# Performance work log

Measured on AMD Instinct MI355X. Metric: run time of the kernel, lower is better.

## Reference

```python
import jax, jax.numpy as jnp
import numpy as np

B, N, D, P = 4, 16384, 128, 100


def setup_inputs() -> dict:
    key = jax.random.key(0)
    k1, k2, k3 = jax.random.split(key, 3)
    x = jax.random.normal(k1, (B, N, D), dtype=jnp.float32)
    y = jax.random.normal(k2, (B, N, D), dtype=jnp.float32)
    thetas = jax.random.normal(k3, (P, D), dtype=jnp.float32)
    return {"x": x, "y": y, "thetas": thetas}


def reference(x, y, thetas):
    # Sliced OT (the branch taken since B*N*N*4 bytes >> memory limit).
    n_proj = thetas.shape[0]
    # F.normalize(theta, dim=0) per projection direction (eps clamp 1e-12)
    norms = jnp.maximum(jnp.linalg.norm(thetas, axis=-1, keepdims=True), 1e-12)
    thetas = thetas / norms  # (P, d)

    # Project all points onto all directions: (P, B, N)
    x_proj = jnp.einsum('bnd,pd->pbn', x, thetas)
    y_proj = jnp.einsum('bnd,pd->pbn', y, thetas)

    # torch: sort y_proj; scatter y_sorted back to original order of x via
    # x_indices = argsort(x_proj). Equivalent: transported_proj[n] =
    # y_sorted[rank_of_x_proj[n]], with rank = argsort(argsort(.)).
    y_sorted = jnp.sort(y_proj, axis=-1)
    ranks = jnp.argsort(jnp.argsort(x_proj, axis=-1), axis=-1)
    transported_proj = jnp.take_along_axis(y_sorted, ranks, axis=-1)  # (P, B, N)

    # Accumulate (transported_proj - x_proj) * theta over projections.
    transported = jnp.einsum('pbn,pd->bnd', transported_proj - x_proj, thetas)
    return x + transported / n_proj
```

## Files before the change

### kernel.cpp

```cpp
#include <hip/hip_runtime.h>
#include <hip/hip_bf16.h>

#define B_    4
#define N_    16384
#define D_    128
#define P_    100
#define BN_   65536
#define PBN_  6553600
#define PPAD  112
#define KPAD  128
#define NBIN  4096

typedef __attribute__((ext_vector_type(8))) short short8;
typedef __attribute__((ext_vector_type(4))) float floatx4;

__device__ __forceinline__ unsigned short f2b(float f) {
    unsigned u = __float_as_uint(f);
    return (unsigned short)((u + 0x7FFFu + ((u >> 16) & 1u)) >> 16);
}
__device__ __forceinline__ float b2f(unsigned short h) {
    return __uint_as_float(((unsigned)h) << 16);
}

__global__ void k_norm(const float* __restrict__ th,
                       unsigned short* __restrict__ thb,
                       unsigned short* __restrict__ thbT) {
    int p = blockIdx.x;
    int d = threadIdx.x;
    float v = 0.f;
    if (p < P_) v = th[p * D_ + d];
    float s = v * v;
    #pragma unroll
    for (int o = 32; o > 0; o >>= 1) s += __shfl_down(s, o, 64);
    __shared__ float red[2];
    if ((d & 63) == 0) red[d >> 6] = s;
    __syncthreads();
    float norm = fmaxf(sqrtf(red[0] + red[1]), 1e-12f);
    unsigned short r = f2b(v / norm);
    if (p < PPAD) thb[p * D_ + d] = r;
    thbT[d * KPAD + p] = r;
}

__global__ __launch_bounds__(256) void k_proj(
    const float* __restrict__ x, const float* __restrict__ y,
    const unsigned short* __restrict__ thb,
    unsigned short* __restrict__ xp, unsigned short* __restrict__ yp) {
    __shared__ unsigned short smem[32640];
    unsigned short* th_s = smem;
    unsigned short* xs   = smem + 15232;
    unsigned short* ys   = xs + 8704;
    unsigned short* bufx = xs;
    unsigned short* bufy = bufx + 8064;
    const int tid  = threadIdx.x;
    const int w    = tid >> 6;
    const int lane = tid & 63;
    const int n    = lane & 15;
    const int quad = lane >> 4;
    const int row0 = blockIdx.x * 64;

    for (int g = tid; g < 1792; g += 256) {
        int r = g >> 4, c = (g & 15) << 3;
        *(uint4*)(th_s + r * 136 + c) = *(const uint4*)(thb + r * D_ + c);
    }
    for (int g = tid; g < 2048; g += 256) {
        int r = g >> 5, c = (g & 31) << 2;
        float4 vx = *(const float4*)(x + (size_t)(row0 + r) * D_ + c);
        float4 vy = *(const float4*)(y + (size_t)(row0 + r) * D_ + c);
        *(ushort4*)(xs + r * 136 + c) =
            make_ushort4(f2b(vx.x), f2b(vx.y), f2b(vx.z), f2b(vx.w));
        *(ushort4*)(ys + r * 136 + c) =
            make_ushort4(f2b(vy.x), f2b(vy.y), f2b(vy.z), f2b(vy.w));
    }
    __syncthreads();

    short8 bx[4], by[4];
    #pragma unroll
    for (int ks = 0; ks < 4; ++ks) {
        bx[ks] = *(const short8*)(xs + (w * 16 + n) * 136 + ks * 32 + quad * 8);
        by[ks] = *(const short8*)(ys + (w * 16 + n) * 136 + ks * 32 + quad * 8);
    }
    __syncthreads();

    #pragma unroll
    for (int pt = 0; pt < 7; ++pt) {
        floatx4 accx = {0.f, 0.f, 0.f, 0.f};
        floatx4 accy = {0.f, 0.f, 0.f, 0.f};
        #pragma unroll
        for (int ks = 0; ks < 4; ++ks) {
            short8 a = *(const short8*)(th_s + (pt * 16 + n) * 136 + ks * 32 + quad * 8);
            accx = __builtin_amdgcn_mfma_f32_16x16x32_bf16(a, bx[ks], accx, 0, 0, 0);
            accy = __builtin_amdgcn_mfma_f32_16x16x32_bf16(a, by[ks], accy, 0, 0, 0);
        }
        #pragma unroll
        for (int reg = 0; reg < 4; ++reg) {
            int p = pt * 16 + quad * 4 + reg;
            bufx[p * 72 + w * 16 + n] = f2b(accx[reg]);
            bufy[p * 72 + w * 16 + n] = f2b(accy[reg]);
        }
    }
    __syncthreads();

    for (int g = tid; g < 896; g += 256) {
        int p = g >> 3, c = (g & 7) << 3;
        *(uint4*)(xp + (size_t)p * BN_ + row0 + c) = *(const uint4*)(bufx + p * 72 + c);
        *(uint4*)(yp + (size_t)p * BN_ + row0 + c) = *(const uint4*)(bufy + p * 72 + c);
    }
}

__device__ __forceinline__ int binof(float v) {
    int k = (int)((v + 8.0f) * 256.0f);
    return k < 0 ? 0 : (k > NBIN - 1 ? NBIN - 1 : k);
}

__device__ __forceinline__ void scan4(unsigned* hist, volatile unsigned* wsum, int t) {
    unsigned v[4], run = 0;
    #pragma unroll
    for (int i = 0; i < 4; ++i) { unsigned h = hist[t * 4 + i]; v[i] = run; run += h; }
    const int lane = t & 63, w = t >> 6;
    unsigned inc = run;
    #pragma unroll
    for (int off = 1; off < 64; off <<= 1) {
        unsigned nbr = __shfl_up(inc, off, 64);
        if (lane >= off) inc += nbr;
    }
    if (lane == 63) wsum[w] = inc;
    __syncthreads();
    if (t == 0) {
        unsigned r2 = 0;
        #pragma unroll
        for (int i = 0; i < 16; ++i) { unsigned h = wsum[i]; wsum[i] = r2; r2 += h; }
    }
    __syncthreads();
    unsigned base = wsum[w] + (inc - run);
    #pragma unroll
    for (int i = 0; i < 4; ++i) hist[t * 4 + i] = base + v[i];
}

__global__ __launch_bounds__(1024, 4) void k_sortdiff(
    const unsigned short* __restrict__ xp, const unsigned short* __restrict__ yp,
    unsigned short* __restrict__ diff) {
    __shared__ unsigned hist[NBIN];
    __shared__ unsigned short ysort[N_];
    __shared__ unsigned wsum[16];
    const size_t base = (size_t)blockIdx.x * N_ + (size_t)threadIdx.x * 16;
    const int t = threadIdx.x;

    unsigned yw[8], xw[8];
    {
        uint4 a = *(const uint4*)(yp + base), b = *(const uint4*)(yp + base + 8);
        yw[0]=a.x; yw[1]=a.y; yw[2]=a.z; yw[3]=a.w;
        yw[4]=b.x; yw[5]=b.y; yw[6]=b.z; yw[7]=b.w;
        uint4 c = *(const uint4*)(xp + base), d = *(const uint4*)(xp + base + 8);
        xw[0]=c.x; xw[1]=c.y; xw[2]=c.z; xw[3]=c.w;
        xw[4]=d.x; xw[5]=d.y; xw[6]=d.z; xw[7]=d.w;
    }

    #pragma unroll
    for (int i = 0; i < 4; ++i) hist[t + i * 1024] = 0;
    __syncthreads();

    unsigned jy[8], jx[8];
    #pragma unroll
    for (int k = 0; k < 8; ++k) {
        unsigned j0 = atomicAdd(&hist[binof(b2f((unsigned short)(yw[k] & 0xffff)))], 1u);
        unsigned j1 = atomicAdd(&hist[binof(b2f((unsigned short)(yw[k] >> 16)))], 1u);
        jy[k] = (j0 & 0xffffu) | (j1 << 16);
        unsigned i0 = atomicAdd(&hist[binof(b2f((unsigned short)(xw[k] & 0xffff)))], 0x10000u);
        unsigned i1 = atomicAdd(&hist[binof(b2f((unsigned short)(xw[k] >> 16)))], 0x10000u);
        jx[k] = (i0 >> 16) | (i1 & 0xffff0000u);
    }
    __syncthreads();
    scan4(hist, wsum, t);
    __syncthreads();

    #pragma unroll
    for (int k = 0; k < 8; ++k) {
        unsigned short e0 = (unsigned short)(yw[k] & 0xffff);
        unsigned short e1 = (unsigned short)(yw[k] >> 16);
        ysort[(hist[binof(b2f(e0))] & 0xffffu) + (jy[k] & 0xffffu)] = e0;
        ysort[(hist[binof(b2f(e1))] & 0xffffu) + (jy[k] >> 16)]     = e1;
        unsigned r0 = (hist[binof(b2f((unsigned short)(xw[k] & 0xffff)))] >> 16) + (jx[k] & 0xffffu);
        unsigned r1 = (hist[binof(b2f((unsigned short)(xw[k] >> 16)))] >> 16) + (jx[k] >> 16);
        jx[k] = r0 | (r1 << 16);
    }
    __syncthreads();

    unsigned ow[8];
    #pragma unroll
    for (int k = 0; k < 8; ++k) {
        float x0 = b2f((unsigned short)(xw[k] & 0xffff));
        float x1 = b2f((unsigned short)(xw[k] >> 16));
        unsigned short d0 = f2b(b2f(ysort[jx[k] & 0xffffu]) - x0);
        unsigned short d1 = f2b(b2f(ysort[jx[k] >> 16]) - x1);
        ow[k] = (unsigned)d0 | ((unsigned)d1 << 16);
    }
    *(uint4*)(diff + base)     = make_uint4(ow[0], ow[1], ow[2], ow[3]);
    *(uint4*)(diff + base + 8) = make_uint4(ow[4], ow[5], ow[6], ow[7]);
}

__global__ __launch_bounds__(256) void k_comb(
    const float* __restrict__ x, const unsigned short* __restrict__ diff,
    const unsigned short* __restrict__ thbT, float* __restrict__ out) {
    __shared__ unsigned short ths[128 * 136];
    __shared__ unsigned Lp[64 * 68];
    const int tid  = threadIdx.x;
    const int w    = tid >> 6;
    const int lane = tid & 63;
    const int n16  = lane & 15;
    const int quad = lane >> 4;
    const int row0 = blockIdx.x * 64;

    for (int g = tid; g < 2048; g += 256) {
        int r = g >> 4, c = (g & 15) << 3;
        *(uint4*)(ths + r * 136 + c) = *(const uint4*)(thbT + r * KPAD + c);
    }
    for (int g = tid; g < 952; g += 256) Lp[50 * 68 + g] = 0;
    for (int g = tid; g < 400; g += 256) {
        int p2 = g >> 3, rg = (g & 7) << 3;
        uint4 a = *(const uint4*)(diff + (size_t)(2 * p2) * BN_ + row0 + rg);
        uint4 b = *(const uint4*)(diff + (size_t)(2 * p2 + 1) * BN_ + row0 + rg);
        unsigned* dst = Lp + p2 * 68 + rg;
        dst[0] = (a.x & 0xffffu) | (b.x << 16);
        dst[1] = (a.x >> 16)     | (b.x & 0xffff0000u);
        dst[2] = (a.y & 0xffffu) | (b.y << 16);
        dst[3] = (a.y >> 16)     | (b.y & 0xffff0000u);
        dst[4] = (a.z & 0xffffu) | (b.z << 16);
        dst[5] = (a.z >> 16)     | (b.z & 0xffff0000u);
        dst[6] = (a.w & 0xffffu) | (b.w << 16);
        dst[7] = (a.w >> 16)     | (b.w & 0xffff0000u);
    }
    __syncthreads();

    const int r = w * 16 + n16;
    short8 af[4];
    #pragma unroll
    for (int ks = 0; ks < 4; ++ks) {
        union { unsigned u[4]; short8 v; } tu;
        #pragma unroll
        for (int m = 0; m < 4; ++m)
            tu.u[m] = Lp[(ks * 16 + quad * 4 + m) * 68 + r];
        af[ks] = tu.v;
    }

    floatx4 acc[8];
    #pragma unroll
    for (int nt = 0; nt < 8; ++nt) {
        acc[nt] = (floatx4){0.f, 0.f, 0.f, 0.f};
        #pragma unroll
        for (int ks = 0; ks < 4; ++ks) {
            short8 b = *(const short8*)(ths + (nt * 16 + n16) * 136 + ks * 32 + quad * 8);
            acc[nt] = __builtin_amdgcn_mfma_f32_16x16x32_bf16(af[ks], b, acc[nt], 0, 0, 0);
        }
    }

    const float invP = 1.0f / (float)P_;
    const size_t rbase = (size_t)(row0 + w * 16 + quad * 4) * D_ + n16;
    #pragma unroll
    for (int nt = 0; nt < 8; ++nt)
        #pragma unroll
        for (int reg = 0; reg < 4; ++reg) {
            size_t o = rbase + (size_t)reg * D_ + nt * 16;
            out[o] = fmaf(acc[nt][reg], invP, x[o]);
        }
}

extern "C" void kernel_launch(void* const* d_in, const int* in_sizes, int n_in,
                              void* d_out, int out_size, void* d_ws, size_t ws_size,
                              hipStream_t stream) {
    const float* x  = (const float*)d_in[0];
    const float* y  = (const float*)d_in[1];
    const float* th = (const float*)d_in[2];
    float* out = (float*)d_out;
    char*  wsb = (char*)d_ws;

    unsigned short* thb  = (unsigned short*)wsb;
    unsigned short* thbT = (unsigned short*)(wsb + 32768);
    unsigned short* xpb  = (unsigned short*)(wsb + 65536);
    unsigned short* ypb  = xpb + PBN_;

    k_norm<<<128, 128, 0, stream>>>(th, thb, thbT);
    k_proj<<<BN_ / 64, 256, 0, stream>>>(x, y, thb, xpb, ypb);
    k_sortdiff<<<P_ * B_, 1024, 0, stream>>>(xpb, ypb, xpb);
    k_comb<<<BN_ / 64, 256, 0, stream>>>(x, xpb, thbT, out);
}
```

Measured before the change: 154.4 us.

## Load projection inputs straight to registers and halve sort block size

k_proj now reads x and y rows directly from global memory into registers in MFMA operand layout, skipping the shared-memory staging pass and its barrier. This shrinks its LDS footprint and adds a two-blocks-per-CU launch bound. k_sortdiff moves from 1024 to 512 threads, with each thread handling 32 elements in coalesced strided chunks and an 8-bin-per-thread scan. The trade-off is more registers per thread and less latency hiding per block in the sort, and uncoalesced-ish row reads in the projection.

```diff
diff --git a/kernel.cpp b/kernel.cpp
--- a/kernel.cpp
+++ b/kernel.cpp
@@ -41,16 +41,13 @@
     thbT[d * KPAD + p] = r;
 }
 
-__global__ __launch_bounds__(256) void k_proj(
+__global__ __launch_bounds__(256, 2) void k_proj(
     const float* __restrict__ x, const float* __restrict__ y,
     const unsigned short* __restrict__ thb,
     unsigned short* __restrict__ xp, unsigned short* __restrict__ yp) {
-    __shared__ unsigned short smem[32640];
-    unsigned short* th_s = smem;
-    unsigned short* xs   = smem + 15232;
-    unsigned short* ys   = xs + 8704;
-    unsigned short* bufx = xs;
-    unsigned short* bufy = bufx + 8064;
+    __shared__ unsigned short th_s[15232];
+    __shared__ unsigned short bufx[8064];
+    __shared__ unsigned short bufy[8064];
     const int tid  = threadIdx.x;
     const int w    = tid >> 6;
     const int lane = tid & 63;
@@ -62,22 +59,30 @@
         int r = g >> 4, c = (g & 15) << 3;
         *(uint4*)(th_s + r * 136 + c) = *(const uint4*)(thb + r * D_ + c);
     }
-    for (int g = tid; g < 2048; g += 256) {
-        int r = g >> 5, c = (g & 31) << 2;
-        float4 vx = *(const float4*)(x + (size_t)(row0 + r) * D_ + c);
-        float4 vy = *(const float4*)(y + (size_t)(row0 + r) * D_ + c);
-        *(ushort4*)(xs + r * 136 + c) =
-            make_ushort4(f2b(vx.x), f2b(vx.y), f2b(vx.z), f2b(vx.w));
-        *(ushort4*)(ys + r * 136 + c) =
-            make_ushort4(f2b(vy.x), f2b(vy.y), f2b(vy.z), f2b(vy.w));
-    }
-    __syncthreads();
-
+
+    const float* xr = x + (size_t)(row0 + w * 16 + n) * D_ + quad * 8;
+    const float* yr = y + (size_t)(row0 + w * 16 + n) * D_ + quad * 8;
+    float4 lx[8], ly[8];
+    #pragma unroll
+    for (int ks = 0; ks < 4; ++ks) {
+        lx[2*ks]   = *(const float4*)(xr + ks * 32);
+        lx[2*ks+1] = *(const float4*)(xr + ks * 32 + 4);
+        ly[2*ks]   = *(const float4*)(yr + ks * 32);
+        ly[2*ks+1] = *(const float4*)(yr + ks * 32 + 4);
+    }
     short8 bx[4], by[4];
     #pragma unroll
     for (int ks = 0; ks < 4; ++ks) {
-        bx[ks] = *(const short8*)(xs + (w * 16 + n) * 136 + ks * 32 + quad * 8);
-        by[ks] = *(const short8*)(ys + (w * 16 + n) * 136 + ks * 32 + quad * 8);
+        short8 tx, ty;
+        tx[0] = (short)f2b(lx[2*ks].x);   ty[0] = (short)f2b(ly[2*ks].x);
+        tx[1] = (short)f2b(lx[2*ks].y);   ty[1] = (short)f2b(ly[2*ks].y);
+        tx[2] = (short)f2b(lx[2*ks].z);   ty[2] = (short)f2b(ly[2*ks].z);
+        tx[3] = (short)f2b(lx[2*ks].w);   ty[3] = (short)f2b(ly[2*ks].w);
+        tx[4] = (short)f2b(lx[2*ks+1].x); ty[4] = (short)f2b(ly[2*ks+1].x);
+        tx[5] = (short)f2b(lx[2*ks+1].y); ty[5] = (short)f2b(ly[2*ks+1].y);
+        tx[6] = (short)f2b(lx[2*ks+1].z); ty[6] = (short)f2b(ly[2*ks+1].z);
+        tx[7] = (short)f2b(lx[2*ks+1].w); ty[7] = (short)f2b(ly[2*ks+1].w);
+        bx[ks] = tx; by[ks] = ty;
     }
     __syncthreads();
 
@@ -112,10 +117,10 @@
     return k < 0 ? 0 : (k > NBIN - 1 ? NBIN - 1 : k);
 }
 
-__device__ __forceinline__ void scan4(unsigned* hist, volatile unsigned* wsum, int t) {
-    unsigned v[4], run = 0;
-    #pragma unroll
-    for (int i = 0; i < 4; ++i) { unsigned h = hist[t * 4 + i]; v[i] = run; run += h; }
+__device__ __forceinline__ void scan8(unsigned* hist, volatile unsigned* wsum, int t) {
+    unsigned v[8], run = 0;
+    #pragma unroll
+    for (int i = 0; i < 8; ++i) { unsigned h = hist[t * 8 + i]; v[i] = run; run += h; }
     const int lane = t & 63, w = t >> 6;
     unsigned inc = run;
     #pragma unroll
@@ -128,40 +133,41 @@
     if (t == 0) {
         unsigned r2 = 0;
         #pragma unroll
-        for (int i = 0; i < 16; ++i) { unsigned h = wsum[i]; wsum[i] = r2; r2 += h; }
+        for (int i = 0; i < 8; ++i) { unsigned h = wsum[i]; wsum[i] = r2; r2 += h; }
     }
     __syncthreads();
     unsigned base = wsum[w] + (inc - run);
     #pragma unroll
-    for (int i = 0; i < 4; ++i) hist[t * 4 + i] = base + v[i];
-}
-
-__global__ __launch_bounds__(1024, 4) void k_sortdiff(
+    for (int i = 0; i < 8; ++i) hist[t * 8 + i] = base + v[i];
+}
+
+__global__ __launch_bounds__(512, 4) void k_sortdiff(
     const unsigned short* __restrict__ xp, const unsigned short* __restrict__ yp,
     unsigned short* __restrict__ diff) {
     __shared__ unsigned hist[NBIN];
     __shared__ unsigned short ysort[N_];
-    __shared__ unsigned wsum[16];
-    const size_t base = (size_t)blockIdx.x * N_ + (size_t)threadIdx.x * 16;
+    __shared__ unsigned wsum[8];
     const int t = threadIdx.x;
-
-    unsigned yw[8], xw[8];
-    {
-        uint4 a = *(const uint4*)(yp + base), b = *(const uint4*)(yp + base + 8);
-        yw[0]=a.x; yw[1]=a.y; yw[2]=a.z; yw[3]=a.w;
-        yw[4]=b.x; yw[5]=b.y; yw[6]=b.z; yw[7]=b.w;
-        uint4 c = *(const uint4*)(xp + base), d = *(const uint4*)(xp + base + 8);
-        xw[0]=c.x; xw[1]=c.y; xw[2]=c.z; xw[3]=c.w;
-        xw[4]=d.x; xw[5]=d.y; xw[6]=d.z; xw[7]=d.w;
-    }
-
-    #pragma unroll
-    for (int i = 0; i < 4; ++i) hist[t + i * 1024] = 0;
-    __syncthreads();
-
-    unsigned jy[8], jx[8];
-    #pragma unroll
-    for (int k = 0; k < 8; ++k) {
+    const unsigned* ypd = (const unsigned*)(yp + (size_t)blockIdx.x * N_);
+    const unsigned* xpd = (const unsigned*)(xp + (size_t)blockIdx.x * N_);
+    unsigned*       dfd = (unsigned*)(diff + (size_t)blockIdx.x * N_);
+
+    unsigned yw[16], xw[16];
+    #pragma unroll
+    for (int i = 0; i < 4; ++i) {
+        uint4 a = *(const uint4*)(ypd + i * 2048 + t * 4);
+        yw[4*i] = a.x; yw[4*i+1] = a.y; yw[4*i+2] = a.z; yw[4*i+3] = a.w;
+        uint4 c = *(const uint4*)(xpd + i * 2048 + t * 4);
+        xw[4*i] = c.x; xw[4*i+1] = c.y; xw[4*i+2] = c.z; xw[4*i+3] = c.w;
+    }
+
+    #pragma unroll
+    for (int i = 0; i < 8; ++i) hist[t + i * 512] = 0;
+    __syncthreads();
+
+    unsigned jy[16], jx[16];
+    #pragma unroll
+    for (int k = 0; k < 16; ++k) {
         unsigned j0 = atomicAdd(&hist[binof(b2f((unsigned short)(yw[k] & 0xffff)))], 1u);
         unsigned j1 = atomicAdd(&hist[binof(b2f((unsigned short)(yw[k] >> 16)))], 1u);
         jy[k] = (j0 & 0xffffu) | (j1 << 16);
@@ -170,11 +176,11 @@
         jx[k] = (i0 >> 16) | (i1 & 0xffff0000u);
     }
     __syncthreads();
-    scan4(hist, wsum, t);
-    __syncthreads();
-
-    #pragma unroll
-    for (int k = 0; k < 8; ++k) {
+    scan8(hist, wsum, t);
+    __syncthreads();
+
+    #pragma unroll
+    for (int k = 0; k < 16; ++k) {
         unsigned short e0 = (unsigned short)(yw[k] & 0xffff);
         unsigned short e1 = (unsigned short)(yw[k] >> 16);
         ysort[(hist[binof(b2f(e0))] & 0xffffu) + (jy[k] & 0xffffu)] = e0;
@@ -185,17 +191,20 @@
     }
     __syncthreads();
 
-    unsigned ow[8];
-    #pragma unroll
-    for (int k = 0; k < 8; ++k) {
-        float x0 = b2f((unsigned short)(xw[k] & 0xffff));
-        float x1 = b2f((unsigned short)(xw[k] >> 16));
-        unsigned short d0 = f2b(b2f(ysort[jx[k] & 0xffffu]) - x0);
-        unsigned short d1 = f2b(b2f(ysort[jx[k] >> 16]) - x1);
-        ow[k] = (unsigned)d0 | ((unsigned)d1 << 16);
-    }
-    *(uint4*)(diff + base)     = make_uint4(ow[0], ow[1], ow[2], ow[3]);
-    *(uint4*)(diff + base + 8) = make_uint4(ow[4], ow[5], ow[6], ow[7]);
+    #pragma unroll
+    for (int i = 0; i < 4; ++i) {
+        unsigned o[4];
+        #pragma unroll
+        for (int q = 0; q < 4; ++q) {
+            int k = 4*i + q;
+            float x0 = b2f((unsigned short)(xw[k] & 0xffff));
+            float x1 = b2f((unsigned short)(xw[k] >> 16));
+            unsigned short d0 = f2b(b2f(ysort[jx[k] & 0xffffu]) - x0);
+            unsigned short d1 = f2b(b2f(ysort[jx[k] >> 16]) - x1);
+            o[q] = (unsigned)d0 | ((unsigned)d1 << 16);
+        }
+        *(uint4*)(dfd + i * 2048 + t * 4) = make_uint4(o[0], o[1], o[2], o[3]);
+    }
 }
 
 __global__ __launch_bounds__(256) void k_comb(
@@ -280,6 +289,6 @@
 
     k_norm<<<128, 128, 0, stream>>>(th, thb, thbT);
     k_proj<<<BN_ / 64, 256, 0, stream>>>(x, y, thb, xpb, ypb);
-    k_sortdiff<<<P_ * B_, 1024, 0, stream>>>(xpb, ypb, xpb);
+    k_sortdiff<<<P_ * B_, 512, 0, stream>>>(xpb, ypb, xpb);
     k_comb<<<BN_ / 64, 256, 0, stream>>>(x, xpb, thbT, out);
 }
```

Result: slower. 176.1 us (+14.1%).
